# Kernel tuning notes

Measured on AMD Instinct MI355X. Metric: run time of the kernel, lower is better.

## Reference

```python
import jax, jax.numpy as jnp
import numpy as np

DIM = 512
DEPTH = 6
HEADS = 8
HD = DIM // HEADS          # head dim = 64
HALF = HD // 4             # rope half_dim = 16
MLP_H = int(DIM * 4.0)
TOKENS = [1, 4, 16, 64]    # CLS, S1, S2, S3
N = sum(TOKENS)            # 85
MAX_FREQ = 10.0
BATCH = 1024
LN_EPS = 1e-5


def _build_mask():
    # CLS sees CLS+S3; each scale sees CLS+itself (block-diagonal + CLS column)
    m = np.full((N, N), -np.inf, dtype=np.float32)
    cum = np.cumsum([0] + TOKENS)  # [0,1,5,21,85]
    m[0, 0] = 0.0
    m[0, cum[3]:cum[4]] = 0.0
    for i in range(1, 4):
        s, e = cum[i], cum[i + 1]
        m[s:e, 0] = 0.0
        m[s:e, s:e] = 0.0
    return jnp.asarray(m)

MASK = _build_mask()
FREQS = jnp.exp(jnp.arange(HALF, dtype=jnp.float32) * (-np.log(MAX_FREQ) / HALF))


def _layer_norm(x, g, b):
    mu = x.mean(-1, keepdims=True)
    var = ((x - mu) ** 2).mean(-1, keepdims=True)
    return (x - mu) * jax.lax.rsqrt(var + LN_EPS) * g + b


def _rope2d(t, coords):
    # t: [B,H,P,HD], coords: [P,2] in [0,1]^2
    ang_x = coords[:, 0:1] * FREQS[None, :] * (2.0 * jnp.pi)  # [P,HALF]
    ang_y = coords[:, 1:2] * FREQS[None, :] * (2.0 * jnp.pi)
    cx, sx = jnp.cos(ang_x), jnp.sin(ang_x)
    cy, sy = jnp.cos(ang_y), jnp.sin(ang_y)
    B, H, P, _ = t.shape
    t = t.reshape(B, H, P, 4, HALF)
    x0, x1, x2, x3 = t[..., 0, :], t[..., 1, :], t[..., 2, :], t[..., 3, :]
    r = jnp.stack([x0 * cx - x1 * sx,
                   x0 * sx + x1 * cx,
                   x2 * cy - x3 * sy,
                   x2 * sy + x3 * cy], axis=3)
    return r.reshape(B, H, P, HD)


def _rope_skip_cls(t, coords):
    return jnp.concatenate([t[:, :, :1], _rope2d(t[:, :, 1:], coords)], axis=2)


def _block(x, coords, p):
    (ln1g, ln1b, qkvw, qkvb, projw, projb,
     ln2g, ln2b, f1w, f1b, f2w, f2b) = p
    B, Nn, D = x.shape
    h = _layer_norm(x, ln1g, ln1b)
    qkv = h @ qkvw + qkvb                         # [B,N,3D]
    qkv = qkv.reshape(B, Nn, 3, HEADS, HD).transpose(2, 0, 3, 1, 4)
    q, k, v = qkv[0], qkv[1], qkv[2]              # [B,H,N,HD]
    q = _rope_skip_cls(q, coords)
    k = _rope_skip_cls(k, coords)
    attn = jnp.einsum('bhqd,bhkd->bhqk', q, k) * (HD ** -0.5) + MASK
    attn = jax.nn.softmax(attn, axis=-1)
    out = jnp.einsum('bhqk,bhkd->bhqd', attn, v)
    out = out.transpose(0, 2, 1, 3).reshape(B, Nn, D)
    x = x + (out @ projw + projb)
    h = _layer_norm(x, ln2g, ln2b)
    h = jax.nn.gelu(h @ f1w + f1b, approximate=False) @ f2w + f2b
    return x + h


def setup_inputs() -> dict:
    key = jax.random.key(0)
    ks = jax.random.split(key, 8)
    s = 0.02
    nrm = lambda k, shape: jax.random.normal(k, shape, jnp.float32) * s
    return dict(
        x=jax.random.normal(ks[0], (BATCH, N, DIM), jnp.float32),
        coords=jax.random.uniform(ks[1], (N - 1, 2), jnp.float32),
        ln1_g=jnp.ones((DEPTH, DIM), jnp.float32),
        ln1_b=jnp.zeros((DEPTH, DIM), jnp.float32),
        qkv_w=nrm(ks[2], (DEPTH, DIM, 3 * DIM)),
        qkv_b=jnp.zeros((DEPTH, 3 * DIM), jnp.float32),
        proj_w=nrm(ks[3], (DEPTH, DIM, DIM)),
        proj_b=jnp.zeros((DEPTH, DIM), jnp.float32),
        ln2_g=jnp.ones((DEPTH, DIM), jnp.float32),
        ln2_b=jnp.zeros((DEPTH, DIM), jnp.float32),
        fc1_w=nrm(ks[4], (DEPTH, DIM, MLP_H)),
        fc1_b=jnp.zeros((DEPTH, MLP_H), jnp.float32),
        fc2_w=nrm(ks[5], (DEPTH, MLP_H, DIM)),
        fc2_b=jnp.zeros((DEPTH, DIM), jnp.float32),
    )


def reference(x, coords, ln1_g, ln1_b, qkv_w, qkv_b, proj_w, proj_b,
              ln2_g, ln2_b, fc1_w, fc1_b, fc2_w, fc2_b):
    for i in range(DEPTH):
        x = _block(x, coords,
                   (ln1_g[i], ln1_b[i], qkv_w[i], qkv_b[i], proj_w[i], proj_b[i],
                    ln2_g[i], ln2_b[i], fc1_w[i], fc1_b[i], fc2_w[i], fc2_b[i]))
    return x
```

## Files before the change

### kernel.cpp

```cpp
#include <hip/hip_runtime.h>
#include <hip/hip_bf16.h>
#include <math.h>

#define DIMX 512
#define NTOK 85
#define BATCH 1024
#define M_ROWS (BATCH * NTOK)
#define MLP_H 2048
#define DEPTH 6

typedef __attribute__((ext_vector_type(8))) short short8;
typedef __attribute__((ext_vector_type(4))) float f32x4;

__device__ inline float bf2f(ushort u) {
    union { unsigned int i; float f; } v; v.i = ((unsigned int)u) << 16; return v.f;
}
__device__ inline ushort f2bf(float f) {
    __hip_bfloat16 h = __float2bfloat16(f);
    union { __hip_bfloat16 h; ushort u; } v; v.h = h; return v.u;
}
__device__ inline unsigned int pack2(float a, float b) {
    return (unsigned int)f2bf(a) | ((unsigned int)f2bf(b) << 16);
}
__device__ inline float gelu_fast(float v) {
    float u = 1.5957691f * fmaf(0.044715f * v, v * v, v);
    return v / (1.0f + __expf(-u));
}

__device__ inline void gload16(const ushort* g, ushort* lds) {
    __builtin_amdgcn_global_load_lds(
        (const __attribute__((address_space(1))) unsigned int*)g,
        (__attribute__((address_space(3))) unsigned int*)lds, 16, 0, 0);
}

__global__ __launch_bounds__(256) void transpose_bf16(const float* __restrict__ in,
                                                      ushort* __restrict__ out,
                                                      int K, int N) {
    __shared__ float tile[32][33];
    int n0 = blockIdx.x * 32, k0 = blockIdx.y * 32;
    int tx = threadIdx.x, ty = threadIdx.y;
    #pragma unroll
    for (int j = 0; j < 32; j += 8)
        tile[ty + j][tx] = in[(size_t)(k0 + ty + j) * N + n0 + tx];
    __syncthreads();
    #pragma unroll
    for (int j = 0; j < 32; j += 8)
        out[(size_t)(n0 + ty + j) * K + k0 + tx] = f2bf(tile[tx][ty + j]);
}

__global__ void rope_table(const float* __restrict__ coords, float* __restrict__ tab) {
    int t = blockIdx.x;
    int idx = threadIdx.x;
    float freq = expf(-(float)idx * (2.302585093f / 16.0f));
    float twopi = 6.283185307179586f;
    float ax = coords[t * 2 + 0] * freq * twopi;
    float ay = coords[t * 2 + 1] * freq * twopi;
    tab[t * 64 + idx]      = cosf(ax);
    tab[t * 64 + 16 + idx] = sinf(ax);
    tab[t * 64 + 32 + idx] = cosf(ay);
    tab[t * 64 + 48 + idx] = sinf(ay);
}

__global__ __launch_bounds__(256) void ln_kernel(const float* __restrict__ x,
                                                 const float* __restrict__ g,
                                                 const float* __restrict__ bta,
                                                 ushort* __restrict__ out) {
    int w = threadIdx.x >> 6, lane = threadIdx.x & 63;
    size_t row = (size_t)blockIdx.x * 4 + w;
    const float* xr = x + row * DIMX;
    int c = lane * 8;
    float4 v0 = *(const float4*)(xr + c);
    float4 v1 = *(const float4*)(xr + c + 4);
    float s = v0.x + v0.y + v0.z + v0.w + v1.x + v1.y + v1.z + v1.w;
    #pragma unroll
    for (int m = 32; m; m >>= 1) s += __shfl_xor(s, m);
    float mu = s * (1.0f / 512.0f);
    float d0 = v0.x - mu, d1 = v0.y - mu, d2 = v0.z - mu, d3 = v0.w - mu;
    float d4 = v1.x - mu, d5 = v1.y - mu, d6 = v1.z - mu, d7 = v1.w - mu;
    float q = d0*d0 + d1*d1 + d2*d2 + d3*d3 + d4*d4 + d5*d5 + d6*d6 + d7*d7;
    #pragma unroll
    for (int m = 32; m; m >>= 1) q += __shfl_xor(q, m);
    float rs = rsqrtf(q * (1.0f / 512.0f) + 1e-5f);
    float4 g0 = *(const float4*)(g + c), g1 = *(const float4*)(g + c + 4);
    float4 b0 = *(const float4*)(bta + c), b1 = *(const float4*)(bta + c + 4);
    uint4 o;
    o.x = pack2(d0 * rs * g0.x + b0.x, d1 * rs * g0.y + b0.y);
    o.y = pack2(d2 * rs * g0.z + b0.z, d3 * rs * g0.w + b0.w);
    o.z = pack2(d4 * rs * g1.x + b1.x, d5 * rs * g1.y + b1.y);
    o.w = pack2(d6 * rs * g1.z + b1.z, d7 * rs * g1.w + b1.w);
    *(uint4*)&out[row * DIMX + c] = o;
}

template <int EPI>
__global__ __launch_bounds__(256, 2) void gemm_wide(const ushort* __restrict__ A,
                                                    const ushort* __restrict__ Bt,
                                                    const float* __restrict__ bias,
                                                    float* __restrict__ outF,
                                                    ushort* __restrict__ outB,
                                                    int M, int N, int K,
                                                    const float* __restrict__ tab) {
    __shared__ ushort As[2][256 * 32] __attribute__((aligned(16)));
    __shared__ ushort Bs[2][128 * 32] __attribute__((aligned(16)));
    int tid = threadIdx.x;
    int w = tid >> 6, lane = tid & 63;
    int wm2 = (w >> 1) * 128;
    int wn = (w & 1) * 64;

    int nbx = gridDim.x;
    int nwg = nbx * gridDim.y;
    int orig = blockIdx.y * nbx + blockIdx.x;
    int q8 = nwg >> 3, r8 = nwg & 7;
    int xcd = orig & 7, loc = orig >> 3;
    int id = (xcd < r8) ? xcd * (q8 + 1) + loc : r8 * (q8 + 1) + (xcd - r8) * q8 + loc;
    int m0 = (id / nbx) * 256;
    int n0 = (id % nbx) * 128;

    int srow = tid >> 2;
    int scol = ((tid & 3) ^ ((srow >> 1) & 3)) * 8;
    const ushort* gAp[4];
    const ushort* gBp[2];
    #pragma unroll
    for (int rn = 0; rn < 4; rn++) {
        int rr2 = m0 + srow + rn * 64; if (rr2 >= M) rr2 = M - 1;
        gAp[rn] = A + (size_t)rr2 * K + scol;
    }
    #pragma unroll
    for (int rn = 0; rn < 2; rn++)
        gBp[rn] = Bt + (size_t)(n0 + srow + rn * 64) * K + scol;
    int dwz = w * 512;

#define STAGEW(T) do { int kc = (T) * 32, sl = (T) & 1;                        \
        gload16(gAp[0] + kc, &As[sl][dwz]);                                    \
        gload16(gAp[1] + kc, &As[sl][2048 + dwz]);                             \
        gload16(gAp[2] + kc, &As[sl][4096 + dwz]);                             \
        gload16(gAp[3] + kc, &As[sl][6144 + dwz]);                             \
        gload16(gBp[0] + kc, &Bs[sl][dwz]);                                    \
        gload16(gBp[1] + kc, &Bs[sl][2048 + dwz]); } while (0)

    int l15 = lane & 15, lq = lane >> 4;
    int sw = (lq ^ ((l15 >> 1) & 3)) * 8;
    int aoff = (wm2 + l15) * 32 + sw;
    int boff = (wn + l15) * 32 + sw;

    int NT = K >> 5;

    STAGEW(0); STAGEW(1);

    f32x4 acc[8][4] = {};

    for (int t = 0; t < NT; ++t) {
        if (t == NT - 1) asm volatile("s_waitcnt vmcnt(0)" ::: "memory");
        else             asm volatile("s_waitcnt vmcnt(6)" ::: "memory");
        __builtin_amdgcn_s_barrier();
        const ushort* sa = As[t & 1];
        const ushort* sb = Bs[t & 1];
        short8 a[8], b[4];
        #pragma unroll
        for (int i = 0; i < 8; i++) a[i] = *(const short8*)&sa[aoff + i * 512];
        #pragma unroll
        for (int j = 0; j < 4; j++) b[j] = *(const short8*)&sb[boff + j * 512];
        asm volatile("s_waitcnt lgkmcnt(0)" ::: "memory");
        __builtin_amdgcn_sched_barrier(0);
        __builtin_amdgcn_s_barrier();
        if (t + 2 < NT) STAGEW(t + 2);
        __builtin_amdgcn_sched_barrier(0);
        __builtin_amdgcn_s_setprio(1);
        #pragma unroll
        for (int i = 0; i < 8; i++)
            #pragma unroll
            for (int j = 0; j < 4; j++)
                acc[i][j] = __builtin_amdgcn_mfma_f32_16x16x32_bf16(a[i], b[j], acc[i][j], 0, 0, 0);
        __builtin_amdgcn_s_setprio(0);
    }
#undef STAGEW

    int cr = lq * 4;
    int cc = l15;
    if (EPI == 0) {
        bool ropeReg = (n0 + wn) < 1024;
        int gnb = n0 + wn + cc;
        float bb0 = bias[gnb], bb1 = bias[gnb + 16], bb2 = bias[gnb + 32], bb3 = bias[gnb + 48];
        #pragma unroll
        for (int i = 0; i < 8; i++) {
            #pragma unroll
            for (int rr = 0; rr < 4; rr++) {
                int gm = m0 + wm2 + i * 16 + cr + rr;
                if (gm >= M) continue;
                int n = gm % NTOK;
                float v0 = acc[i][0][rr] + bb0;
                float v1 = acc[i][1][rr] + bb1;
                float v2 = acc[i][2][rr] + bb2;
                float v3 = acc[i][3][rr] + bb3;
                if (ropeReg && n > 0) {
                    const float* tt = tab + (size_t)(n - 1) * 64 + cc;
                    float cx = tt[0], sx = tt[16], cy = tt[32], sy = tt[48];
                    float y0 = v0 * cx - v1 * sx;
                    float y1 = v0 * sx + v1 * cx;
                    float y2 = v2 * cy - v3 * sy;
                    float y3 = v2 * sy + v3 * cy;
                    v0 = y0; v1 = y1; v2 = y2; v3 = y3;
                }
                size_t o = (size_t)gm * N + gnb;
                outB[o]      = f2bf(v0);
                outB[o + 16] = f2bf(v1);
                outB[o + 32] = f2bf(v2);
                outB[o + 48] = f2bf(v3);
            }
        }
    } else {
        #pragma unroll
        for (int i = 0; i < 8; i++) {
            #pragma unroll
            for (int rr = 0; rr < 4; rr++) {
                int gm = m0 + wm2 + i * 16 + cr + rr;
                if (gm >= M) continue;
                #pragma unroll
                for (int j = 0; j < 4; j++) {
                    int gn = n0 + wn + j * 16 + cc;
                    float v = acc[i][j][rr] + bias[gn];
                    size_t o = (size_t)gm * N + gn;
                    if (EPI == 1) {
                        outF[o] = outF[o] + v;
                    } else {
                        outB[o] = f2bf(gelu_fast(v));
                    }
                }
            }
        }
    }
}

__global__ __launch_bounds__(384) void attn_kernel(const ushort* __restrict__ qkv,
                                                   ushort* __restrict__ out) {
    __shared__ ushort SU[13824] __attribute__((aligned(16)));
    __shared__ ushort Vt[6656]  __attribute__((aligned(16)));
    int bh = blockIdx.x;
    int b = bh >> 3, h = bh & 7;
    int tid = threadIdx.x;
    size_t base = (size_t)b * NTOK * 1536 + h * 64;

    for (int it = tid; it < 1536; it += 384) {
        int mat = (it >= 768) ? 1 : 0;
        int item = it - mat * 768;
        int n = item >> 3, g = item & 7;
        short8 v = {};
        if (n < NTOK)
            v = *(const short8*)&qkv[base + (size_t)n * 1536 + mat * 512 + g * 8];
        *(short8*)&SU[mat * 6912 + n * 72 + g * 8] = v;
    }
    for (int it = tid; it < 768; it += 384) {
        int n = it % 96;
        int d0 = (it / 96) * 8;
        short8 v = {};
        if (n < NTOK)
            v = *(const short8*)&qkv[base + (size_t)n * 1536 + 1024 + d0];
        #pragma unroll
        for (int j = 0; j < 8; j++)
            Vt[(d0 + j) * 104 + n] = (ushort)v[j];
    }
    __syncthreads();

    int wid = tid >> 6;
    int lane = tid & 63;
    int q = lane >> 4, c = lane & 15;
    int i0 = wid * 16;

    f32x4 acc[6] = {};
    #pragma unroll
    for (int kk = 0; kk < 2; kk++) {
        short8 aq = *(const short8*)&SU[(i0 + c) * 72 + kk * 32 + q * 8];
        #pragma unroll
        for (int t = 0; t < 6; t++) {
            short8 bk = *(const short8*)&SU[6912 + (t * 16 + c) * 72 + kk * 32 + q * 8];
            acc[t] = __builtin_amdgcn_mfma_f32_16x16x32_bf16(aq, bk, acc[t], 0, 0, 0);
        }
    }
    __syncthreads();

    #pragma unroll
    for (int r = 0; r < 4; r++) {
        int i = i0 + q * 4 + r;
        int si = (i == 0) ? 3 : (i < 5 ? 1 : (i < 21 ? 2 : 3));
        float vs[6];
        float m = -1e30f;
        #pragma unroll
        for (int t = 0; t < 6; t++) {
            int j = t * 16 + c;
            int sj = (j == 0) ? si : (j < 5 ? 1 : (j < 21 ? 2 : (j < NTOK ? 3 : -1)));
            float v = (sj == si) ? acc[t][r] * 0.125f : -1e30f;
            vs[t] = v;
            m = fmaxf(m, v);
        }
        #pragma unroll
        for (int mk = 8; mk; mk >>= 1) m = fmaxf(m, __shfl_xor(m, mk));
        float s = 0.f, ps[6];
        #pragma unroll
        for (int t = 0; t < 6; t++) { ps[t] = __expf(vs[t] - m); s += ps[t]; }
        #pragma unroll
        for (int mk = 8; mk; mk >>= 1) s += __shfl_xor(s, mk);
        float inv = 1.0f / s;
        #pragma unroll
        for (int t = 0; t < 6; t++)
            SU[i * 104 + t * 16 + c] = f2bf(ps[t] * inv);
    }
    __syncthreads();

    f32x4 o2[4] = {};
    #pragma unroll
    for (int kk = 0; kk < 3; kk++) {
        short8 ap = *(const short8*)&SU[(i0 + c) * 104 + kk * 32 + q * 8];
        #pragma unroll
        for (int nt = 0; nt < 4; nt++) {
            short8 bv = *(const short8*)&Vt[(nt * 16 + c) * 104 + kk * 32 + q * 8];
            o2[nt] = __builtin_amdgcn_mfma_f32_16x16x32_bf16(ap, bv, o2[nt], 0, 0, 0);
        }
    }
    size_t orow = (size_t)b * NTOK;
    #pragma unroll
    for (int nt = 0; nt < 4; nt++) {
        #pragma unroll
        for (int r = 0; r < 4; r++) {
            int i = i0 + q * 4 + r;
            if (i < NTOK)
                out[(orow + i) * DIMX + h * 64 + nt * 16 + c] = f2bf(o2[nt][r]);
        }
    }
}

extern "C" void kernel_launch(void* const* d_in, const int* in_sizes, int n_in,
                              void* d_out, int out_size, void* d_ws, size_t ws_size,
                              hipStream_t stream) {
    const float* x_in    = (const float*)d_in[0];
    const float* coords  = (const float*)d_in[1];
    const float* ln1_g   = (const float*)d_in[2];
    const float* ln1_b   = (const float*)d_in[3];
    const float* qkv_w   = (const float*)d_in[4];
    const float* qkv_b   = (const float*)d_in[5];
    const float* proj_w  = (const float*)d_in[6];
    const float* proj_b  = (const float*)d_in[7];
    const float* ln2_g   = (const float*)d_in[8];
    const float* ln2_b   = (const float*)d_in[9];
    const float* fc1_w   = (const float*)d_in[10];
    const float* fc1_b   = (const float*)d_in[11];
    const float* fc2_w   = (const float*)d_in[12];
    const float* fc2_b   = (const float*)d_in[13];

    char* ws = (char*)d_ws;
    size_t off = 0;
    auto alloc = [&](size_t bytes) -> void* {
        void* p = ws + off;
        off += (bytes + 255) & ~(size_t)255;
        return p;
    };
    auto asz = [](size_t b) { return (b + 255) & ~(size_t)255; };

    const size_t WPL = 512 * 1536 + 512 * 512 + 512 * 2048 + 2048 * 512;

    size_t fixed = asz(WPL * DEPTH * sizeof(ushort)) + asz(84 * 64 * sizeof(float));
    int Bc = 1024;
    while (Bc > 4) {
        size_t rc = (size_t)Bc * NTOK;
        size_t need = fixed + asz(rc * DIMX * sizeof(ushort)) + asz(rc * MLP_H * sizeof(ushort));
        if (need <= ws_size) break;
        Bc >>= 1;
    }
    size_t Rc = (size_t)Bc * NTOK;

    ushort* wt   = (ushort*)alloc(WPL * DEPTH * sizeof(ushort));
    float*  tab  = (float*)alloc(84 * 64 * sizeof(float));
    ushort* hbuf = (ushort*)alloc(Rc * DIMX * sizeof(ushort));
    ushort* big  = (ushort*)alloc(Rc * MLP_H * sizeof(ushort));

    hipMemcpyAsync(d_out, x_in, (size_t)M_ROWS * DIMX * sizeof(float),
                   hipMemcpyDeviceToDevice, stream);

    rope_table<<<84, 16, 0, stream>>>(coords, tab);

    dim3 tb(32, 8);
    for (int l = 0; l < DEPTH; l++) {
        ushort* wl = wt + (size_t)l * WPL;
        transpose_bf16<<<dim3(1536 / 32, 512 / 32), tb, 0, stream>>>(
            qkv_w + (size_t)l * 512 * 1536, wl, 512, 1536);
        transpose_bf16<<<dim3(512 / 32, 512 / 32), tb, 0, stream>>>(
            proj_w + (size_t)l * 512 * 512, wl + 786432, 512, 512);
        transpose_bf16<<<dim3(2048 / 32, 512 / 32), tb, 0, stream>>>(
            fc1_w + (size_t)l * 512 * 2048, wl + 1048576, 512, 2048);
        transpose_bf16<<<dim3(512 / 32, 2048 / 32), tb, 0, stream>>>(
            fc2_w + (size_t)l * 2048 * 512, wl + 2097152, 2048, 512);
    }

    int mt256 = (int)(Rc / 256);
    int lnblocks = (int)(Rc / 4);
    for (int c = 0; c < BATCH / Bc; c++) {
        float* xc = (float*)d_out + (size_t)c * Rc * DIMX;
        int Mc = (int)Rc;
        for (int l = 0; l < DEPTH; l++) {
            ushort* wl = wt + (size_t)l * WPL;
            ln_kernel<<<lnblocks, 256, 0, stream>>>(
                xc, ln1_g + l * 512, ln1_b + l * 512, hbuf);
            gemm_wide<0><<<dim3(1536 / 128, mt256), 256, 0, stream>>>(
                hbuf, wl, qkv_b + (size_t)l * 1536, nullptr, big, Mc, 1536, 512, tab);
            attn_kernel<<<Bc * 8, 384, 0, stream>>>(big, hbuf);
            gemm_wide<1><<<dim3(512 / 128, mt256), 256, 0, stream>>>(
                hbuf, wl + 786432, proj_b + (size_t)l * 512, xc, nullptr,
                Mc, 512, 512, nullptr);
            ln_kernel<<<lnblocks, 256, 0, stream>>>(
                xc, ln2_g + l * 512, ln2_b + l * 512, hbuf);
            gemm_wide<2><<<dim3(2048 / 128, mt256), 256, 0, stream>>>(
                hbuf, wl + 1048576, fc1_b + (size_t)l * 2048, nullptr, big,
                Mc, 2048, 512, nullptr);
            gemm_wide<1><<<dim3(512 / 128, mt256), 256, 0, stream>>>(
                big, wl + 2097152, fc2_b + (size_t)l * 512, xc, nullptr,
                Mc, 512, 2048, nullptr);
        }
    }
}
```

Measured before the change: 7.220 ms.

## Triple-buffer LDS tiles in wide GEMM and drop second barrier per k-step

Shared-memory staging for the wide GEMM goes from two buffers to three, with rotating offsets and incrementing global pointers. With a third buffer, the next prefetch can be issued right after the LDS fragment reads, and the second workgroup barrier in each k-iteration is removed. This targets barrier stalls and load/compute serialization, at the cost of 50% more LDS, which may limit occupancy at two workgroups per CU.

Measured after the change: 7.141 ms. About the same (-1.1%).

```diff
diff --git a/kernel.cpp b/kernel.cpp
--- a/kernel.cpp
+++ b/kernel.cpp
@@ -99,8 +99,8 @@
                                                     ushort* __restrict__ outB,
                                                     int M, int N, int K,
                                                     const float* __restrict__ tab) {
-    __shared__ ushort As[2][256 * 32] __attribute__((aligned(16)));
-    __shared__ ushort Bs[2][128 * 32] __attribute__((aligned(16)));
+    __shared__ ushort AsF[3 * 8192] __attribute__((aligned(16)));
+    __shared__ ushort BsF[3 * 4096] __attribute__((aligned(16)));
     int tid = threadIdx.x;
     int w = tid >> 6, lane = tid & 63;
     int wm2 = (w >> 1) * 128;
@@ -117,52 +117,53 @@
 
     int srow = tid >> 2;
     int scol = ((tid & 3) ^ ((srow >> 1) & 3)) * 8;
-    const ushort* gAp[4];
-    const ushort* gBp[2];
-    #pragma unroll
-    for (int rn = 0; rn < 4; rn++) {
-        int rr2 = m0 + srow + rn * 64; if (rr2 >= M) rr2 = M - 1;
-        gAp[rn] = A + (size_t)rr2 * K + scol;
-    }
-    #pragma unroll
-    for (int rn = 0; rn < 2; rn++)
-        gBp[rn] = Bt + (size_t)(n0 + srow + rn * 64) * K + scol;
+    int rA0 = m0 + srow;       if (rA0 >= M) rA0 = M - 1;
+    int rA1 = m0 + 64 + srow;  if (rA1 >= M) rA1 = M - 1;
+    int rA2 = m0 + 128 + srow; if (rA2 >= M) rA2 = M - 1;
+    int rA3 = m0 + 192 + srow; if (rA3 >= M) rA3 = M - 1;
+    const ushort* gA0 = A + (size_t)rA0 * K + scol;
+    const ushort* gA1 = A + (size_t)rA1 * K + scol;
+    const ushort* gA2 = A + (size_t)rA2 * K + scol;
+    const ushort* gA3 = A + (size_t)rA3 * K + scol;
+    const ushort* gB0 = Bt + (size_t)(n0 + srow) * K + scol;
+    const ushort* gB1 = Bt + (size_t)(n0 + 64 + srow) * K + scol;
     int dwz = w * 512;
-
-#define STAGEW(T) do { int kc = (T) * 32, sl = (T) & 1;                        \
-        gload16(gAp[0] + kc, &As[sl][dwz]);                                    \
-        gload16(gAp[1] + kc, &As[sl][2048 + dwz]);                             \
-        gload16(gAp[2] + kc, &As[sl][4096 + dwz]);                             \
-        gload16(gAp[3] + kc, &As[sl][6144 + dwz]);                             \
-        gload16(gBp[0] + kc, &Bs[sl][dwz]);                                    \
-        gload16(gBp[1] + kc, &Bs[sl][2048 + dwz]); } while (0)
+    int swA = 0, swB = 0;
+
+#define STAGEW() do {                                                          \
+        gload16(gA0, &AsF[swA + dwz]);                                         \
+        gload16(gA1, &AsF[swA + 2048 + dwz]);                                  \
+        gload16(gA2, &AsF[swA + 4096 + dwz]);                                  \
+        gload16(gA3, &AsF[swA + 6144 + dwz]);                                  \
+        gload16(gB0, &BsF[swB + dwz]);                                         \
+        gload16(gB1, &BsF[swB + 2048 + dwz]);                                  \
+        gA0 += 32; gA1 += 32; gA2 += 32; gA3 += 32; gB0 += 32; gB1 += 32;      \
+        swA += 8192; if (swA == 24576) swA = 0;                                \
+        swB += 4096; if (swB == 12288) swB = 0; } while (0)
 
     int l15 = lane & 15, lq = lane >> 4;
     int sw = (lq ^ ((l15 >> 1) & 3)) * 8;
     int aoff = (wm2 + l15) * 32 + sw;
     int boff = (wn + l15) * 32 + sw;
+    int roffA = 0, roffB = 0;
 
     int NT = K >> 5;
 
-    STAGEW(0); STAGEW(1);
+    STAGEW(); STAGEW();
 
     f32x4 acc[8][4] = {};
 
     for (int t = 0; t < NT; ++t) {
-        if (t == NT - 1) asm volatile("s_waitcnt vmcnt(0)" ::: "memory");
-        else             asm volatile("s_waitcnt vmcnt(6)" ::: "memory");
+        if (t < NT - 1) asm volatile("s_waitcnt vmcnt(6)" ::: "memory");
+        else            asm volatile("s_waitcnt vmcnt(0)" ::: "memory");
         __builtin_amdgcn_s_barrier();
-        const ushort* sa = As[t & 1];
-        const ushort* sb = Bs[t & 1];
         short8 a[8], b[4];
         #pragma unroll
-        for (int i = 0; i < 8; i++) a[i] = *(const short8*)&sa[aoff + i * 512];
-        #pragma unroll
-        for (int j = 0; j < 4; j++) b[j] = *(const short8*)&sb[boff + j * 512];
+        for (int i = 0; i < 8; i++) a[i] = *(const short8*)&AsF[roffA + aoff + i * 512];
+        #pragma unroll
+        for (int j = 0; j < 4; j++) b[j] = *(const short8*)&BsF[roffB + boff + j * 512];
+        if (t + 2 < NT) STAGEW();
         asm volatile("s_waitcnt lgkmcnt(0)" ::: "memory");
-        __builtin_amdgcn_sched_barrier(0);
-        __builtin_amdgcn_s_barrier();
-        if (t + 2 < NT) STAGEW(t + 2);
         __builtin_amdgcn_sched_barrier(0);
         __builtin_amdgcn_s_setprio(1);
         #pragma unroll
@@ -171,6 +172,8 @@
             for (int j = 0; j < 4; j++)
                 acc[i][j] = __builtin_amdgcn_mfma_f32_16x16x32_bf16(a[i], b[j], acc[i][j], 0, 0, 0);
         __builtin_amdgcn_s_setprio(0);
+        roffA += 8192; if (roffA == 24576) roffA = 0;
+        roffB += 4096; if (roffB == 12288) roffB = 0;
     }
 #undef STAGEW
 
```
